# Performance work log

Hardware: AMD Instinct MI355X
Metric: run time of the kernel (lower is better)

## Reference

```python
import jax, jax.numpy as jnp
import numpy as np

H = 8
D_MODEL = 512
D_K = D_MODEL // H


def setup_inputs() -> dict:
    key = jax.random.key(0)
    ks = jax.random.split(key, 12)
    B, S = 4, 2048
    scale = 1.0 / np.sqrt(D_MODEL)
    inp = {
        "query": jax.random.normal(ks[0], (B, S, D_MODEL), jnp.float32),
        "key": jax.random.normal(ks[1], (B, S, D_MODEL), jnp.float32),
        "value": jax.random.normal(ks[2], (B, S, D_MODEL), jnp.float32),
        "mask": jnp.ones((B, 1, S), jnp.int32),
        "Wq": jax.random.normal(ks[3], (D_MODEL, D_MODEL), jnp.float32) * scale,
        "bq": jax.random.normal(ks[4], (D_MODEL,), jnp.float32) * 0.01,
        "Wk": jax.random.normal(ks[5], (D_MODEL, D_MODEL), jnp.float32) * scale,
        "bk": jax.random.normal(ks[6], (D_MODEL,), jnp.float32) * 0.01,
        "Wv": jax.random.normal(ks[7], (D_MODEL, D_MODEL), jnp.float32) * scale,
        "bv": jax.random.normal(ks[8], (D_MODEL,), jnp.float32) * 0.01,
        "Wo": jax.random.normal(ks[9], (D_MODEL, D_MODEL), jnp.float32) * scale,
        "bo": jax.random.normal(ks[10], (D_MODEL,), jnp.float32) * 0.01,
    }
    return inp


def reference(query, key, value, mask, Wq, bq, Wk, bk, Wv, bv, Wo, bo):
    B, S, _ = query.shape

    def proj(x, W, b):
        # [B,S,D] -> [B,H,S,d_k]
        y = jnp.einsum('bsd,ed->bse', x, W) + b  # torch Linear: x @ W.T + b
        return y.reshape(B, S, H, D_K).transpose(0, 2, 1, 3)

    q = proj(query, Wq, bq)
    k = proj(key, Wk, bk)
    v = proj(value, Wv, bv)

    scores = jnp.einsum('bhqd,bhkd->bhqk', q, k) / jnp.sqrt(jnp.float32(D_K))
    m = mask[:, None, :, :]  # [B,1,1,S]
    scores = jnp.where(m == 0, jnp.float32(-1e9), scores)
    p_attn = jax.nn.softmax(scores, axis=-1)  # dropout is identity in eval
    x = jnp.einsum('bhqk,bhkd->bhqd', p_attn, v)
    x = x.transpose(0, 2, 1, 3).reshape(B, S, D_MODEL)
    return jnp.einsum('bsd,ed->bse', x, Wo) + bo
```

## Files before the change

kernel.cpp:

```cpp
#include <hip/hip_runtime.h>
#include <hip/hip_bf16.h>

#define H 8
#define DMODEL 512
#define DK 64
#define BATCH 4
#define SEQ 2048
#define M_TOTAL (BATCH*SEQ)

typedef short bf16x8 __attribute__((ext_vector_type(8)));
typedef float f32x4 __attribute__((ext_vector_type(4)));

__device__ __forceinline__ unsigned short f2bf(float f) {
    unsigned int u = __builtin_bit_cast(unsigned int, f);
    u += 0x7FFFu + ((u >> 16) & 1u);
    return (unsigned short)(u >> 16);
}

__device__ __forceinline__ unsigned int pack_bf2(float a, float b) {
    unsigned int r;
    asm("v_cvt_pk_bf16_f32 %0, %1, %2" : "=v"(r) : "v"(a), "v"(b));
    return r;
}

__device__ __forceinline__ float exp2_fast(float x) {
    float r;
    asm("v_exp_f32 %0, %1" : "=v"(r) : "v"(x));
    return r;
}

__global__ __launch_bounds__(256) void gemm_qkv(
    const float* __restrict__ query, const float* __restrict__ key_,
    const float* __restrict__ value,
    const float* __restrict__ Wq, const float* __restrict__ bq,
    const float* __restrict__ Wk, const float* __restrict__ bk,
    const float* __restrict__ Wv, const float* __restrict__ bv,
    unsigned short* __restrict__ Qh, unsigned short* __restrict__ Kh,
    unsigned short* __restrict__ Vt)
{
    const int z = blockIdx.z;
    const float* A    = (z == 0) ? query : (z == 1) ? key_ : value;
    const float* W    = (z == 0) ? Wq : (z == 1) ? Wk : Wv;
    const float* bias = (z == 0) ? bq : (z == 1) ? bk : bv;
    unsigned short* out = (z == 0) ? Qh : (z == 1) ? Kh : Vt;

    const int m0 = blockIdx.x * 128;
    const int n0 = blockIdx.y * 64;
    const int tid = threadIdx.x;
    const int lane = tid & 63;
    const int w = tid >> 6;
    const int g = lane >> 4, qi = lane & 15;
    const int wm = w >> 1, wn = w & 1;

    __shared__ unsigned short Alds[128 * 40];
    __shared__ unsigned short Blds[64 * 40];

    f32x4 acc[4][2];
    #pragma unroll
    for (int i = 0; i < 4; i++)
        #pragma unroll
        for (int j = 0; j < 2; j++) acc[i][j] = f32x4{0.f, 0.f, 0.f, 0.f};

    float4 aA[4], bA[2], aB[4], bB[2];

    auto ld = [&](float4 (&ar)[4], float4 (&br)[2], int k0) {
        #pragma unroll
        for (int i = 0; i < 4; i++) { int idx = tid + i * 256;
            ar[i] = *(const float4*)(A + (size_t)(m0 + (idx >> 3)) * 512 + k0 + (idx & 7) * 4); }
        #pragma unroll
        for (int i = 0; i < 2; i++) { int idx = tid + i * 256;
            br[i] = *(const float4*)(W + (size_t)(n0 + (idx >> 3)) * 512 + k0 + (idx & 7) * 4); }
    };
    auto st = [&](float4 (&ar)[4], float4 (&br)[2]) {
        #pragma unroll
        for (int i = 0; i < 4; i++) { int idx = tid + i * 256;
            uint2 p; p.x = pack_bf2(ar[i].x, ar[i].y); p.y = pack_bf2(ar[i].z, ar[i].w);
            *(uint2*)(Alds + (idx >> 3) * 40 + (idx & 7) * 4) = p; }
        #pragma unroll
        for (int i = 0; i < 2; i++) { int idx = tid + i * 256;
            uint2 p; p.x = pack_bf2(br[i].x, br[i].y); p.y = pack_bf2(br[i].z, br[i].w);
            *(uint2*)(Blds + (idx >> 3) * 40 + (idx & 7) * 4) = p; }
    };
    auto tile = [&]() {
        bf16x8 af[4], bf[2];
        #pragma unroll
        for (int mt = 0; mt < 4; mt++)
            af[mt] = *(const bf16x8*)(Alds + (wm * 64 + mt * 16 + qi) * 40 + g * 8);
        #pragma unroll
        for (int nt = 0; nt < 2; nt++)
            bf[nt] = *(const bf16x8*)(Blds + (wn * 32 + nt * 16 + qi) * 40 + g * 8);
        #pragma unroll
        for (int mt = 0; mt < 4; mt++)
            #pragma unroll
            for (int nt = 0; nt < 2; nt++)
                acc[mt][nt] = __builtin_amdgcn_mfma_f32_16x16x32_bf16(af[mt], bf[nt], acc[mt][nt], 0, 0, 0);
    };

    ld(aA, bA, 0);
    for (int k0 = 0; k0 < 512; k0 += 64) {
        __syncthreads();
        st(aA, bA);
        ld(aB, bB, k0 + 32);
        __syncthreads();
        tile();
        __syncthreads();
        st(aB, bB);
        if (k0 + 64 < 512) ld(aA, bA, k0 + 64);
        __syncthreads();
        tile();
    }

    #pragma unroll
    for (int mt = 0; mt < 4; mt++) {
        int mbase = m0 + wm * 64 + mt * 16 + g * 4;
        #pragma unroll
        for (int nt = 0; nt < 2; nt++) {
            int n = n0 + wn * 32 + nt * 16 + qi;
            float bv = bias[n];
            int h = n >> 6, dk = n & 63;
            if (z == 2) {
                int b = mbase >> 11, s = mbase & 2047;
                uint2 pk;
                pk.x = pack_bf2(acc[mt][nt][0] + bv, acc[mt][nt][1] + bv);
                pk.y = pack_bf2(acc[mt][nt][2] + bv, acc[mt][nt][3] + bv);
                *(uint2*)(out + ((size_t)(b * H + h) * 64 + dk) * SEQ + s) = pk;
            } else {
                float sc = (z == 0) ? 0.18033688011112042f : 1.0f;
                #pragma unroll
                for (int r = 0; r < 4; r++) {
                    int m = mbase + r;
                    int b = m >> 11, s = m & 2047;
                    out[((size_t)(b * H + h) * SEQ + s) * 64 + dk] = f2bf((acc[mt][nt][r] + bv) * sc);
                }
            }
        }
    }
}

__global__ __launch_bounds__(256) void gemm_o(
    const unsigned short* __restrict__ Xa, const float* __restrict__ W,
    const float* __restrict__ bias, float* __restrict__ out)
{
    const int m0 = blockIdx.x * 128;
    const int n0 = blockIdx.y * 64;
    const int tid = threadIdx.x;
    const int lane = tid & 63;
    const int w = tid >> 6;
    const int g = lane >> 4, qi = lane & 15;
    const int wm = w >> 1, wn = w & 1;

    __shared__ unsigned short Alds[128 * 40];
    __shared__ unsigned short Blds[64 * 40];

    f32x4 acc[4][2];
    #pragma unroll
    for (int i = 0; i < 4; i++)
        #pragma unroll
        for (int j = 0; j < 2; j++) acc[i][j] = f32x4{0.f, 0.f, 0.f, 0.f};

    bf16x8 aA[2], aB[2];
    float4 bA[2], bB[2];

    auto ld = [&](bf16x8 (&ar)[2], float4 (&br)[2], int k0) {
        #pragma unroll
        for (int i = 0; i < 2; i++) { int idx = tid + i * 256;
            ar[i] = *(const bf16x8*)(Xa + (size_t)(m0 + (idx >> 2)) * 512 + k0 + (idx & 3) * 8); }
        #pragma unroll
        for (int i = 0; i < 2; i++) { int idx = tid + i * 256;
            br[i] = *(const float4*)(W + (size_t)(n0 + (idx >> 3)) * 512 + k0 + (idx & 7) * 4); }
    };
    auto st = [&](bf16x8 (&ar)[2], float4 (&br)[2]) {
        #pragma unroll
        for (int i = 0; i < 2; i++) { int idx = tid + i * 256;
            *(bf16x8*)(Alds + (idx >> 2) * 40 + (idx & 3) * 8) = ar[i]; }
        #pragma unroll
        for (int i = 0; i < 2; i++) { int idx = tid + i * 256;
            uint2 p; p.x = pack_bf2(br[i].x, br[i].y); p.y = pack_bf2(br[i].z, br[i].w);
            *(uint2*)(Blds + (idx >> 3) * 40 + (idx & 7) * 4) = p; }
    };
    auto tile = [&]() {
        bf16x8 af[4], bf[2];
        #pragma unroll
        for (int mt = 0; mt < 4; mt++)
            af[mt] = *(const bf16x8*)(Alds + (wm * 64 + mt * 16 + qi) * 40 + g * 8);
        #pragma unroll
        for (int nt = 0; nt < 2; nt++)
            bf[nt] = *(const bf16x8*)(Blds + (wn * 32 + nt * 16 + qi) * 40 + g * 8);
        #pragma unroll
        for (int mt = 0; mt < 4; mt++)
            #pragma unroll
            for (int nt = 0; nt < 2; nt++)
                acc[mt][nt] = __builtin_amdgcn_mfma_f32_16x16x32_bf16(af[mt], bf[nt], acc[mt][nt], 0, 0, 0);
    };

    ld(aA, bA, 0);
    for (int k0 = 0; k0 < 512; k0 += 64) {
        __syncthreads();
        st(aA, bA);
        ld(aB, bB, k0 + 32);
        __syncthreads();
        tile();
        __syncthreads();
        st(aB, bB);
        if (k0 + 64 < 512) ld(aA, bA, k0 + 64);
        __syncthreads();
        tile();
    }

    #pragma unroll
    for (int mt = 0; mt < 4; mt++) {
        int mbase = m0 + wm * 64 + mt * 16 + g * 4;
        #pragma unroll
        for (int nt = 0; nt < 2; nt++) {
            int n = n0 + wn * 32 + nt * 16 + qi;
            float bv = bias[n];
            #pragma unroll
            for (int r = 0; r < 4; r++)
                out[(size_t)(mbase + r) * 512 + n] = acc[mt][nt][r] + bv;
        }
    }
}

__global__ __launch_bounds__(512, 4) void attn_kernel(
    const unsigned short* __restrict__ Qh,
    const unsigned short* __restrict__ Kh,
    const unsigned short* __restrict__ Vt,
    const int* __restrict__ mask,
    unsigned short* __restrict__ Xattn)
{
    const int tid = threadIdx.x;
    const int lane = tid & 63;
    const int w = tid >> 6;
    const int g = lane >> 4;
    const int qi = lane & 15;
    const int s3 = qi & 7;

    const int bid = blockIdx.x;
    const int xcd = bid & 7;
    const int slot = bid >> 3;
    const int bh = xcd * 4 + (slot >> 4);
    const int q0 = (slot & 15) * 128;
    const int b = bh >> 3;

    __shared__ unsigned short Klds[3][64 * 64];
    __shared__ unsigned short Vlds[3][64 * 64];
    __shared__ unsigned short Plds[8][16 * 64];
    __shared__ int amflag;

    bf16x8 qf0, qf1;
    {
        const unsigned short* Qbase =
            Qh + ((size_t)bh * SEQ + q0 + w * 16 + qi) * 64 + g * 8;
        qf0 = *(const bf16x8*)(Qbase);
        qf1 = *(const bf16x8*)(Qbase + 32);
    }

    f32x4 acc_o[4];
    #pragma unroll
    for (int dt = 0; dt < 4; dt++) acc_o[dt] = f32x4{0.f, 0.f, 0.f, 0.f};
    float l_lane = 0.f;

    const unsigned char* Kbh = (const unsigned char*)(Kh + (size_t)bh * SEQ * 64);
    const unsigned char* Vbh = (const unsigned char*)(Vt + (size_t)bh * 64 * SEQ);
    const int* maskb = mask + b * SEQ;

    if (tid == 0) amflag = 1;
    __syncthreads();
    {
        int v = 1;
        #pragma unroll
        for (int i = 0; i < 4; i++) v &= (maskb[tid + i * 512] != 0) ? 1 : 0;
        if (__ballot(v != 0) != ~0ull && lane == 0) amflag = 0;
    }
    __syncthreads();
    const bool allmask = (amflag != 0);

    const int klane = ((lane >> 3) << 7)  + (((lane & 7) ^ (lane >> 3)) << 4);
    const int vlane = ((lane >> 3) << 12) + (((lane & 7) ^ (lane >> 3)) << 4);

    const int rb0 = qi * 128 + ((g ^ s3) << 4);
    unsigned char* Pw = (unsigned char*)&Plds[w][0];
    const int pw0 = qi * 128 + (((g >> 1) ^ s3) << 4) + ((g & 1) << 3);

    auto stage = [&](const unsigned char* ks, const unsigned char* vs, int buf) {
        unsigned char* kd = (unsigned char*)&Klds[buf][0];
        unsigned char* vd = (unsigned char*)&Vlds[buf][0];
        const int c = w;
        __builtin_amdgcn_global_load_lds(
            (const __attribute__((address_space(1))) unsigned int*)(ks + c * 1024),
            (__attribute__((address_space(3))) unsigned int*)(kd + c * 1024), 16, 0, 0);
        __builtin_amdgcn_global_load_lds(
            (const __attribute__((address_space(1))) unsigned int*)(vs + c * 32768),
            (__attribute__((address_space(3))) unsigned int*)(vd + c * 1024), 16, 0, 0);
    };

    auto compute = [&](int t, int buf) {
        const int kv0 = t << 6;
        const unsigned char* KB = (const unsigned char*)&Klds[buf][0];
        const unsigned char* VB = (const unsigned char*)&Vlds[buf][0];

        f32x4 sacc[4];
        __builtin_amdgcn_s_setprio(1);
        #pragma unroll
        for (int nt = 0; nt < 4; nt++) {
            bf16x8 kf0 = *(const bf16x8*)(KB + (rb0 ^ 0)  + nt * 2048);
            bf16x8 kf1 = *(const bf16x8*)(KB + (rb0 ^ 64) + nt * 2048);
            f32x4 sa = f32x4{0.f, 0.f, 0.f, 0.f};
            sa = __builtin_amdgcn_mfma_f32_16x16x32_bf16(kf0, qf0, sa, 0, 0, 0);
            sa = __builtin_amdgcn_mfma_f32_16x16x32_bf16(kf1, qf1, sa, 0, 0, 0);
            sacc[nt] = sa;
        }
        __builtin_amdgcn_s_setprio(0);

        if (!allmask) {
            const unsigned long long mb = __ballot(maskb[kv0 + lane] != 0);
            if (mb != ~0ull) {
                #pragma unroll
                for (int nt = 0; nt < 4; nt++)
                    #pragma unroll
                    for (int r = 0; r < 4; r++) {
                        int kvl = nt * 16 + g * 4 + r;
                        if (!((mb >> kvl) & 1ull)) sacc[nt][r] = -1e9f;
                    }
            }
        }

        #pragma unroll
        for (int nt = 0; nt < 4; nt++) {
            float p0 = exp2_fast(sacc[nt][0]);
            float p1 = exp2_fast(sacc[nt][1]);
            float p2 = exp2_fast(sacc[nt][2]);
            float p3 = exp2_fast(sacc[nt][3]);
            l_lane += (p0 + p1) + (p2 + p3);
            uint2 pk;
            pk.x = pack_bf2(p0, p1);
            pk.y = pack_bf2(p2, p3);
            *(uint2*)(Pw + (pw0 ^ (nt << 5))) = pk;
        }

        __builtin_amdgcn_s_setprio(1);
        #pragma unroll
        for (int kt = 0; kt < 2; kt++) {
            bf16x8 pf = *(const bf16x8*)(Pw + (rb0 ^ (kt << 6)));
            #pragma unroll
            for (int dt = 0; dt < 4; dt++) {
                bf16x8 vf = *(const bf16x8*)(VB + (rb0 ^ (kt << 6)) + dt * 2048);
                acc_o[dt] = __builtin_amdgcn_mfma_f32_16x16x32_bf16(vf, pf, acc_o[dt], 0, 0, 0);
            }
        }
        __builtin_amdgcn_s_setprio(0);
    };

    const unsigned char* ks = Kbh + klane;
    const unsigned char* vs = Vbh + vlane;

    stage(ks, vs, 0); ks += 8192; vs += 128;
    stage(ks, vs, 1); ks += 8192; vs += 128;
    int bc = 0, bs = 2;
    #pragma unroll 1
    for (int t = 0; t < 32; ++t) {
        if (t < 31) __builtin_amdgcn_s_waitcnt(0xF72);
        else        __builtin_amdgcn_s_waitcnt(0xF70);
        __builtin_amdgcn_s_barrier();
        compute(t, bc);
        if (t + 2 < 32) {
            stage(ks, vs, bs);
            ks += 8192; vs += 128;
        }
        bc = (bc == 2) ? 0 : bc + 1;
        bs = (bs == 2) ? 0 : bs + 1;
    }

    const int h = bh & 7;
    float l = l_lane;
    l += __shfl_xor(l, 16);
    l += __shfl_xor(l, 32);
    const float inv = 1.0f / l;
    const int s = q0 + w * 16 + qi;
    size_t base = ((size_t)b * SEQ + s) * 512 + h * 64;
    #pragma unroll
    for (int dt = 0; dt < 4; dt++) {
        uint2 o;
        o.x = pack_bf2(acc_o[dt][0] * inv, acc_o[dt][1] * inv);
        o.y = pack_bf2(acc_o[dt][2] * inv, acc_o[dt][3] * inv);
        *(uint2*)(Xattn + base + dt * 16 + g * 4) = o;
    }
}

extern "C" void kernel_launch(void* const* d_in, const int* in_sizes, int n_in,
                              void* d_out, int out_size, void* d_ws, size_t ws_size,
                              hipStream_t stream)
{
    const float* query = (const float*)d_in[0];
    const float* key_  = (const float*)d_in[1];
    const float* value = (const float*)d_in[2];
    const int*   mask  = (const int*)d_in[3];
    const float* Wq = (const float*)d_in[4];
    const float* bq = (const float*)d_in[5];
    const float* Wk = (const float*)d_in[6];
    const float* bk = (const float*)d_in[7];
    const float* Wv = (const float*)d_in[8];
    const float* bv = (const float*)d_in[9];
    const float* Wo = (const float*)d_in[10];
    const float* bo = (const float*)d_in[11];

    unsigned short* Qh = (unsigned short*)d_ws;
    unsigned short* Kh = Qh + (size_t)M_TOTAL * DMODEL;
    unsigned short* Vt = Kh + (size_t)M_TOTAL * DMODEL;
    unsigned short* Xa = Vt + (size_t)M_TOTAL * DMODEL;

    hipLaunchKernelGGL(gemm_qkv, dim3(64, 8, 3), dim3(256), 0, stream,
                       query, key_, value, Wq, bq, Wk, bk, Wv, bv, Qh, Kh, Vt);
    hipLaunchKernelGGL(attn_kernel, dim3(512), dim3(512), 0, stream, Qh, Kh, Vt, mask, Xa);
    hipLaunchKernelGGL(gemm_o, dim3(64, 8), dim3(256), 0, stream, Xa, Wo, bo, (float*)d_out);
}
```

Baseline: 90.27 us.

## Switch attention to 32x32x16 MFMA with register-resident P via permlane32 swap

Rewrites the attention inner loop to use 32x32x16 bf16 MFMAs with 4 waves of 32 query rows each instead of 8 waves of 16 rows. The softmax probabilities are rearranged in registers with v_permlane32_swap so they feed the PV MFMA directly, which removes the per-wave P round trip through LDS and its shared buffer. This cuts LDS traffic and instruction count but doubles the per-wave accumulator and register footprint, and halves threads per block, which may lower occupancy.

```diff
diff --git a/kernel.cpp b/kernel.cpp
--- a/kernel.cpp
+++ b/kernel.cpp
@@ -10,6 +10,7 @@
 
 typedef short bf16x8 __attribute__((ext_vector_type(8)));
 typedef float f32x4 __attribute__((ext_vector_type(4)));
+typedef float f32x16 __attribute__((ext_vector_type(16)));
 
 __device__ __forceinline__ unsigned short f2bf(float f) {
     unsigned int u = __builtin_bit_cast(unsigned int, f);
@@ -27,6 +28,13 @@
     float r;
     asm("v_exp_f32 %0, %1" : "=v"(r) : "v"(x));
     return r;
+}
+
+__device__ __forceinline__ f32x16 zero16() {
+    f32x16 z;
+    #pragma unroll
+    for (int i = 0; i < 16; i++) z[i] = 0.f;
+    return z;
 }
 
 __global__ __launch_bounds__(256) void gemm_qkv(
@@ -221,7 +229,7 @@
     }
 }
 
-__global__ __launch_bounds__(512, 4) void attn_kernel(
+__global__ __launch_bounds__(256, 2) void attn_kernel(
     const unsigned short* __restrict__ Qh,
     const unsigned short* __restrict__ Kh,
     const unsigned short* __restrict__ Vt,
@@ -231,9 +239,9 @@
     const int tid = threadIdx.x;
     const int lane = tid & 63;
     const int w = tid >> 6;
-    const int g = lane >> 4;
-    const int qi = lane & 15;
-    const int s3 = qi & 7;
+    const int c = lane & 31;
+    const int hi = lane >> 5;
+    const int x7 = lane & 7;
 
     const int bid = blockIdx.x;
     const int xcd = bid & 7;
@@ -244,20 +252,20 @@
 
     __shared__ unsigned short Klds[3][64 * 64];
     __shared__ unsigned short Vlds[3][64 * 64];
-    __shared__ unsigned short Plds[8][16 * 64];
     __shared__ int amflag;
 
-    bf16x8 qf0, qf1;
+    bf16x8 qfr[4];
     {
         const unsigned short* Qbase =
-            Qh + ((size_t)bh * SEQ + q0 + w * 16 + qi) * 64 + g * 8;
-        qf0 = *(const bf16x8*)(Qbase);
-        qf1 = *(const bf16x8*)(Qbase + 32);
-    }
-
-    f32x4 acc_o[4];
-    #pragma unroll
-    for (int dt = 0; dt < 4; dt++) acc_o[dt] = f32x4{0.f, 0.f, 0.f, 0.f};
+            Qh + ((size_t)bh * SEQ + q0 + w * 32 + c) * 64 + hi * 8;
+        #pragma unroll
+        for (int seg = 0; seg < 4; seg++)
+            qfr[seg] = *(const bf16x8*)(Qbase + seg * 16);
+    }
+
+    f32x16 acc[2];
+    acc[0] = zero16();
+    acc[1] = zero16();
     float l_lane = 0.f;
 
     const unsigned char* Kbh = (const unsigned char*)(Kh + (size_t)bh * SEQ * 64);
@@ -269,7 +277,7 @@
     {
         int v = 1;
         #pragma unroll
-        for (int i = 0; i < 4; i++) v &= (maskb[tid + i * 512] != 0) ? 1 : 0;
+        for (int i = 0; i < 8; i++) v &= (maskb[tid + i * 256] != 0) ? 1 : 0;
         if (__ballot(v != 0) != ~0ull && lane == 0) amflag = 0;
     }
     __syncthreads();
@@ -278,77 +286,84 @@
     const int klane = ((lane >> 3) << 7)  + (((lane & 7) ^ (lane >> 3)) << 4);
     const int vlane = ((lane >> 3) << 12) + (((lane & 7) ^ (lane >> 3)) << 4);
 
-    const int rb0 = qi * 128 + ((g ^ s3) << 4);
-    unsigned char* Pw = (unsigned char*)&Plds[w][0];
-    const int pw0 = qi * 128 + (((g >> 1) ^ s3) << 4) + ((g & 1) << 3);
+    const int krow = c * 128;
 
     auto stage = [&](const unsigned char* ks, const unsigned char* vs, int buf) {
         unsigned char* kd = (unsigned char*)&Klds[buf][0];
         unsigned char* vd = (unsigned char*)&Vlds[buf][0];
-        const int c = w;
-        __builtin_amdgcn_global_load_lds(
-            (const __attribute__((address_space(1))) unsigned int*)(ks + c * 1024),
-            (__attribute__((address_space(3))) unsigned int*)(kd + c * 1024), 16, 0, 0);
-        __builtin_amdgcn_global_load_lds(
-            (const __attribute__((address_space(1))) unsigned int*)(vs + c * 32768),
-            (__attribute__((address_space(3))) unsigned int*)(vd + c * 1024), 16, 0, 0);
+        #pragma unroll
+        for (int j = 0; j < 2; j++) {
+            const int cc = w + 4 * j;
+            __builtin_amdgcn_global_load_lds(
+                (const __attribute__((address_space(1))) unsigned int*)(ks + cc * 1024),
+                (__attribute__((address_space(3))) unsigned int*)(kd + cc * 1024), 16, 0, 0);
+            __builtin_amdgcn_global_load_lds(
+                (const __attribute__((address_space(1))) unsigned int*)(vs + cc * 32768),
+                (__attribute__((address_space(3))) unsigned int*)(vd + cc * 1024), 16, 0, 0);
+        }
     };
 
     auto compute = [&](int t, int buf) {
-        const int kv0 = t << 6;
         const unsigned char* KB = (const unsigned char*)&Klds[buf][0];
         const unsigned char* VB = (const unsigned char*)&Vlds[buf][0];
-
-        f32x4 sacc[4];
-        __builtin_amdgcn_s_setprio(1);
-        #pragma unroll
-        for (int nt = 0; nt < 4; nt++) {
-            bf16x8 kf0 = *(const bf16x8*)(KB + (rb0 ^ 0)  + nt * 2048);
-            bf16x8 kf1 = *(const bf16x8*)(KB + (rb0 ^ 64) + nt * 2048);
-            f32x4 sa = f32x4{0.f, 0.f, 0.f, 0.f};
-            sa = __builtin_amdgcn_mfma_f32_16x16x32_bf16(kf0, qf0, sa, 0, 0, 0);
-            sa = __builtin_amdgcn_mfma_f32_16x16x32_bf16(kf1, qf1, sa, 0, 0, 0);
-            sacc[nt] = sa;
-        }
-        __builtin_amdgcn_s_setprio(0);
-
-        if (!allmask) {
-            const unsigned long long mb = __ballot(maskb[kv0 + lane] != 0);
+        const int kv0 = t << 6;
+
+        unsigned long long mb = ~0ull;
+        if (!allmask) mb = __ballot(maskb[kv0 + lane] != 0);
+
+        #pragma unroll
+        for (int kt = 0; kt < 2; kt++) {
+            f32x16 sa = zero16();
+            __builtin_amdgcn_s_setprio(1);
+            #pragma unroll
+            for (int seg = 0; seg < 4; seg++) {
+                bf16x8 kf = *(const bf16x8*)(
+                    KB + kt * 4096 + krow + ((((seg << 1) | hi) ^ x7) << 4));
+                sa = __builtin_amdgcn_mfma_f32_32x32x16_bf16(kf, qfr[seg], sa, 0, 0, 0);
+            }
+            __builtin_amdgcn_s_setprio(0);
+
             if (mb != ~0ull) {
                 #pragma unroll
-                for (int nt = 0; nt < 4; nt++)
-                    #pragma unroll
-                    for (int r = 0; r < 4; r++) {
-                        int kvl = nt * 16 + g * 4 + r;
-                        if (!((mb >> kvl) & 1ull)) sacc[nt][r] = -1e9f;
-                    }
+                for (int r = 0; r < 16; r++) {
+                    int kvl = (r & 3) + 8 * (r >> 2) + 4 * hi + 32 * kt;
+                    if (!((mb >> kvl) & 1ull)) sa[r] = -1e9f;
+                }
             }
-        }
-
-        #pragma unroll
-        for (int nt = 0; nt < 4; nt++) {
-            float p0 = exp2_fast(sacc[nt][0]);
-            float p1 = exp2_fast(sacc[nt][1]);
-            float p2 = exp2_fast(sacc[nt][2]);
-            float p3 = exp2_fast(sacc[nt][3]);
-            l_lane += (p0 + p1) + (p2 + p3);
-            uint2 pk;
-            pk.x = pack_bf2(p0, p1);
-            pk.y = pack_bf2(p2, p3);
-            *(uint2*)(Pw + (pw0 ^ (nt << 5))) = pk;
-        }
-
-        __builtin_amdgcn_s_setprio(1);
-        #pragma unroll
-        for (int kt = 0; kt < 2; kt++) {
-            bf16x8 pf = *(const bf16x8*)(Pw + (rb0 ^ (kt << 6)));
-            #pragma unroll
-            for (int dt = 0; dt < 4; dt++) {
-                bf16x8 vf = *(const bf16x8*)(VB + (rb0 ^ (kt << 6)) + dt * 2048);
-                acc_o[dt] = __builtin_amdgcn_mfma_f32_16x16x32_bf16(vf, pf, acc_o[dt], 0, 0, 0);
+
+            float pe[16];
+            #pragma unroll
+            for (int r = 0; r < 16; r++) pe[r] = exp2_fast(sa[r]);
+            l_lane += (((pe[0] + pe[1]) + (pe[2] + pe[3])) +
+                       ((pe[4] + pe[5]) + (pe[6] + pe[7]))) +
+                      (((pe[8] + pe[9]) + (pe[10] + pe[11])) +
+                       ((pe[12] + pe[13]) + (pe[14] + pe[15])));
+
+            unsigned int a0 = pack_bf2(pe[0],  pe[1]),  a1 = pack_bf2(pe[2],  pe[3]);
+            unsigned int b0 = pack_bf2(pe[4],  pe[5]),  b1 = pack_bf2(pe[6],  pe[7]);
+            unsigned int c0 = pack_bf2(pe[8],  pe[9]),  c1 = pack_bf2(pe[10], pe[11]);
+            unsigned int d0 = pack_bf2(pe[12], pe[13]), d1 = pack_bf2(pe[14], pe[15]);
+            asm("v_permlane32_swap_b32 %0, %1" : "+v"(a0), "+v"(b0));
+            asm("v_permlane32_swap_b32 %0, %1" : "+v"(a1), "+v"(b1));
+            asm("v_permlane32_swap_b32 %0, %1" : "+v"(c0), "+v"(d0));
+            asm("v_permlane32_swap_b32 %0, %1" : "+v"(c1), "+v"(d1));
+            uint4 u0 = {a0, a1, b0, b1};
+            uint4 u1 = {c0, c1, d0, d1};
+            bf16x8 pf0 = __builtin_bit_cast(bf16x8, u0);
+            bf16x8 pf1 = __builtin_bit_cast(bf16x8, u1);
+
+            __builtin_amdgcn_s_setprio(1);
+            #pragma unroll
+            for (int dt = 0; dt < 2; dt++) {
+                bf16x8 vf0 = *(const bf16x8*)(
+                    VB + dt * 4096 + krow + ((((kt << 2) | 0 | hi) ^ x7) << 4));
+                acc[dt] = __builtin_amdgcn_mfma_f32_32x32x16_bf16(vf0, pf0, acc[dt], 0, 0, 0);
+                bf16x8 vf1 = *(const bf16x8*)(
+                    VB + dt * 4096 + krow + ((((kt << 2) | 2 | hi) ^ x7) << 4));
+                acc[dt] = __builtin_amdgcn_mfma_f32_32x32x16_bf16(vf1, pf1, acc[dt], 0, 0, 0);
             }
-        }
-        __builtin_amdgcn_s_setprio(0);
+            __builtin_amdgcn_s_setprio(0);
+        }
     };
 
     const unsigned char* ks = Kbh + klane;
@@ -359,7 +374,7 @@
     int bc = 0, bs = 2;
     #pragma unroll 1
     for (int t = 0; t < 32; ++t) {
-        if (t < 31) __builtin_amdgcn_s_waitcnt(0xF72);
+        if (t < 31) __builtin_amdgcn_s_waitcnt(0xF74);
         else        __builtin_amdgcn_s_waitcnt(0xF70);
         __builtin_amdgcn_s_barrier();
         compute(t, bc);
@@ -372,18 +387,20 @@
     }
 
     const int h = bh & 7;
-    float l = l_lane;
-    l += __shfl_xor(l, 16);
-    l += __shfl_xor(l, 32);
+    float l = l_lane + __shfl_xor(l_lane, 32);
     const float inv = 1.0f / l;
-    const int s = q0 + w * 16 + qi;
+    const int s = q0 + w * 32 + c;
     size_t base = ((size_t)b * SEQ + s) * 512 + h * 64;
     #pragma unroll
-    for (int dt = 0; dt < 4; dt++) {
-        uint2 o;
-        o.x = pack_bf2(acc_o[dt][0] * inv, acc_o[dt][1] * inv);
-        o.y = pack_bf2(acc_o[dt][2] * inv, acc_o[dt][3] * inv);
-        *(uint2*)(Xattn + base + dt * 16 + g * 4) = o;
+    for (int dt = 0; dt < 2; dt++) {
+        #pragma unroll
+        for (int rg = 0; rg < 4; rg++) {
+            const int d0i = rg * 8 + hi * 4 + dt * 32;
+            uint2 o;
+            o.x = pack_bf2(acc[dt][4 * rg]     * inv, acc[dt][4 * rg + 1] * inv);
+            o.y = pack_bf2(acc[dt][4 * rg + 2] * inv, acc[dt][4 * rg + 3] * inv);
+            *(uint2*)(Xattn + base + d0i) = o;
+        }
     }
 }
 
@@ -411,6 +428,6 @@
 
     hipLaunchKernelGGL(gemm_qkv, dim3(64, 8, 3), dim3(256), 0, stream,
                        query, key_, value, Wq, bq, Wk, bk, Wv, bv, Qh, Kh, Vt);
-    hipLaunchKernelGGL(attn_kernel, dim3(512), dim3(512), 0, stream, Qh, Kh, Vt, mask, Xa);
+    hipLaunchKernelGGL(attn_kernel, dim3(512), dim3(256), 0, stream, Qh, Kh, Vt, mask, Xa);
     hipLaunchKernelGGL(gemm_o, dim3(64, 8), dim3(256), 0, stream, Xa, Wo, bo, (float*)d_out);
 }
```

Result: no change. 89.92 us (-0.4%).
